# Performance work log

Measured on AMD Instinct MI355X. Metric: run time of the kernel, lower is better.

## Reference

```python
import jax, jax.numpy as jnp
import numpy as np

NUM_HEADS = 4
WINDOW = 7
DILATION = 1
NEG_MIN = jnp.finfo(jnp.float32).min


def _offsets():
    r = WINDOW // 2
    return [(i - r) * DILATION for i in range(WINDOW)]


def _gather_neighbors(x):
    # x: [B, C, H, W] -> [B, C, K, H, W] with zero padding outside bounds.
    B, C, H, W = x.shape
    offs = _offsets()
    r = (WINDOW // 2) * DILATION
    xp = jnp.pad(x, ((0, 0), (0, 0), (r, r), (r, r)))
    slices = [xp[:, :, r + dy:r + dy + H, r + dx:r + dx + W]
              for dy in offs for dx in offs]
    return jnp.stack(slices, axis=2)


def _valid_mask(H, W):
    # [K, H, W] bool: neighbor (h+dy, w+dx) is inside the image.
    offs = _offsets()
    hh = jnp.arange(H)[:, None]
    ww = jnp.arange(W)[None, :]
    masks = [((hh + dy >= 0) & (hh + dy < H) & (ww + dx >= 0) & (ww + dx < W))
             for dy in offs for dx in offs]
    return jnp.stack(masks, axis=0)


def setup_inputs() -> dict:
    key = jax.random.key(0)
    k1, k2, k3 = jax.random.split(key, 3)
    shape = (2, 64, 96, 96)
    return {
        "q": jax.random.normal(k1, shape, dtype=jnp.float32),
        "k": jax.random.normal(k2, shape, dtype=jnp.float32),
        "v": jax.random.normal(k3, shape, dtype=jnp.float32),
    }


def reference(q, k, v):
    B, C, H, W = q.shape
    d_head = C // NUM_HEADS
    K = WINDOW * WINDOW

    q_heads = q.reshape(B, NUM_HEADS, d_head, H, W)
    k_nb = _gather_neighbors(k).reshape(B, NUM_HEADS, d_head, K, H, W)
    v_nb = _gather_neighbors(v).reshape(B, NUM_HEADS, d_head, K, H, W)
    # [B, heads, K, d_head, H, W]
    k_nb = jnp.transpose(k_nb, (0, 1, 3, 2, 4, 5))
    v_nb = jnp.transpose(v_nb, (0, 1, 3, 2, 4, 5))

    scale = 1.0 / jnp.sqrt(jnp.float32(d_head))
    scores = jnp.einsum('bhdyx,bhkdyx->bhkyx', q_heads, k_nb) * scale
    mask = _valid_mask(H, W)[None, None]  # [1,1,K,H,W]
    scores = jnp.where(mask, scores, NEG_MIN)
    attn = jax.nn.softmax(scores, axis=2)
    out = jnp.einsum('bhkyx,bhkdyx->bhdyx', attn, v_nb)
    return out.reshape(B, C, H, W)
```

## Files before the change

### kernel.cpp

```cpp
#include <hip/hip_runtime.h>

#define HH 96
#define WW 96
#define CH 64
#define NHEADS 4
#define DHEAD 16
#define BATCH 2
#define PLANE (HH * WW)

#define BROWS 6
#define BCOLS 16
#define HROWS (BROWS + 6)
#define HCOLS 24
#define KPITCH 20
#define KPIX (HROWS * HCOLS)
#define KPIXA (KPIX + 8)
#define VPITCH HCOLS
#define VCH (HROWS * VPITCH + 8)
#define TY_N (HH / BROWS)
#define TX_N (WW / BCOLS)

typedef _Float16 half4 __attribute__((ext_vector_type(4)));
typedef _Float16 h2 __attribute__((ext_vector_type(2)));
typedef float f32x4 __attribute__((ext_vector_type(4)));

__device__ __forceinline__ half4 pack4(float a, float b, float c, float d) {
#if __has_builtin(__builtin_amdgcn_cvt_pkrtz)
    h2 lo = __builtin_bit_cast(h2, __builtin_amdgcn_cvt_pkrtz(a, b));
    h2 hi = __builtin_bit_cast(h2, __builtin_amdgcn_cvt_pkrtz(c, d));
    half4 r; r.x = lo.x; r.y = lo.y; r.z = hi.x; r.w = hi.y;
    return r;
#else
    half4 r; r.x = (_Float16)a; r.y = (_Float16)b;
    r.z = (_Float16)c; r.w = (_Float16)d;
    return r;
#endif
}

template <bool INTERIOR>
__device__ __forceinline__ void block_body(
    const float* __restrict__ q, const float* __restrict__ k,
    const float* __restrict__ v, float* __restrict__ out,
    _Float16* __restrict__ lk, _Float16* __restrict__ lv,
    int c0, int h0, int w0)
{
    const int tid = threadIdx.x;

    const int lane = tid & 63;
    const int wid  = tid >> 6;
    const int lp   = lane & 15;
    const int lg   = lane >> 4;
    const int h    = h0 + wid;

    const float QS = 0.25f * 1.4426950408889634f;
    const int qbase = (c0 + lg * 4) * PLANE + h * WW + w0 + lp;
    half4 qf;
    qf.x = (_Float16)(q[qbase] * QS);
    qf.y = (_Float16)(q[qbase + PLANE] * QS);
    qf.z = (_Float16)(q[qbase + 2 * PLANE] * QS);
    qf.w = (_Float16)(q[qbase + 3 * PLANE] * QS);

    const int l16  = tid & 15;
    const int grp  = tid >> 4;
    const int col0 = l16 * 2;
    const bool act = (col0 < HCOLS);

    if constexpr (INTERIOR) {
        float2 kb[8];
#pragma unroll
        for (int r = 0; r < 8; ++r) {
            const int sid = r * 24 + grp;
            const int row = sid >> 4, ch = sid & 15;
            if (act)
                kb[r] = *(const float2*)(k + (size_t)(c0 + ch) * PLANE +
                                         (h0 - 3 + row) * WW + (w0 - 4) + col0);
        }
#pragma unroll
        for (int r = 0; r < 8; ++r) {
            const int sid = r * 24 + grp;
            const int row = sid >> 4, ch = sid & 15;
            if (act) {
                const int pix = row * HCOLS + col0;
                lk[pix * KPITCH + ch]       = (_Float16)kb[r].x;
                lk[(pix + 1) * KPITCH + ch] = (_Float16)kb[r].y;
            }
        }
        float2 vb[8];
#pragma unroll
        for (int r = 0; r < 8; ++r) {
            const int sid = r * 24 + grp;
            const int row = sid >> 4, ch = sid & 15;
            if (act)
                vb[r] = *(const float2*)(v + (size_t)(c0 + ch) * PLANE +
                                         (h0 - 3 + row) * WW + (w0 - 4) + col0);
        }
#pragma unroll
        for (int r = 0; r < 8; ++r) {
            const int sid = r * 24 + grp;
            const int row = sid >> 4, ch = sid & 15;
            if (act) {
                h2 t; t.x = (_Float16)vb[r].x; t.y = (_Float16)vb[r].y;
                *(h2*)&lv[ch * VCH + row * VPITCH + col0] = t;
            }
        }
    } else {
#pragma unroll
        for (int r = 0; r < 8; ++r) {
            const int sid = r * 24 + grp;
            const int row = sid >> 4, ch = sid & 15;
            if (act) {
                const int gh = min(max(h0 - 3 + row, 0), HH - 1);
                const int ga = min(max(w0 - 4 + col0, 0), WW - 1);
                const int gb = min(max(w0 - 3 + col0, 0), WW - 1);
                const float* p0 = k + (size_t)(c0 + ch) * PLANE + gh * WW;
                const int pix = row * HCOLS + col0;
                lk[pix * KPITCH + ch]       = (_Float16)p0[ga];
                lk[(pix + 1) * KPITCH + ch] = (_Float16)p0[gb];
            }
        }
#pragma unroll
        for (int r = 0; r < 8; ++r) {
            const int sid = r * 24 + grp;
            const int row = sid >> 4, ch = sid & 15;
            if (act) {
                const int gh = min(max(h0 - 3 + row, 0), HH - 1);
                const int ga = min(max(w0 - 4 + col0, 0), WW - 1);
                const int gb = min(max(w0 - 3 + col0, 0), WW - 1);
                const float* p0 = v + (size_t)(c0 + ch) * PLANE + gh * WW;
                h2 t; t.x = (_Float16)p0[ga]; t.y = (_Float16)p0[gb];
                *(h2*)&lv[ch * VCH + row * VPITCH + col0] = t;
            }
        }
    }

    {
        h2 z; z.x = (_Float16)0.f; z.y = (_Float16)0.f;
        if (tid < 80)
            *(h2*)&lk[KPIX * KPITCH + tid * 2] = z;
        if (tid < 64)
            *(h2*)&lv[(tid >> 2) * VCH + HROWS * VPITCH + (tid & 3) * 2] = z;
    }
    __syncthreads();

    bool ok1[4], ok2[4];
#pragma unroll
    for (int e = 0; e < 4; ++e) {
        const int j1 = lg * 4 + e;
        const int j2 = 16 + j1;
        ok1[e] = ((unsigned)(j1 - lp - 1) < 7u);
        ok2[e] = ((unsigned)(j2 - lp - 1) < 7u);
        if constexpr (!INTERIOR) {
            ok1[e] = ok1[e] && ((unsigned)(w0 - 4 + j1) < (unsigned)WW);
            ok2[e] = ok2[e] && ((unsigned)(w0 - 4 + j2) < (unsigned)WW);
        }
    }

    f32x4 accA = {0.f, 0.f, 0.f, 0.f};
    f32x4 accB = {0.f, 0.f, 0.f, 0.f};
    float ssA = 0.f, ssB = 0.f;

#pragma unroll
    for (int dy = 0; dy < 7; ++dy) {
        if constexpr (!INTERIOR) {
            if ((unsigned)(h + dy - 3) >= (unsigned)HH) continue;
        }
        const int r = wid + dy;

        const half4 ka1 = *(const half4*)&lk[(r * HCOLS + lp) * KPITCH + lg * 4];
        const half4 ka2 = *(const half4*)&lk[(r * HCOLS + 16 + lp) * KPITCH + lg * 4];
        const f32x4 zz = {0.f, 0.f, 0.f, 0.f};
        f32x4 s1 = __builtin_amdgcn_mfma_f32_16x16x16f16(ka1, qf, zz, 0, 0, 0);
        f32x4 s2 = __builtin_amdgcn_mfma_f32_16x16x16f16(ka2, qf, zz, 0, 0, 0);

        const float e10 = ok1[0] ? __builtin_amdgcn_exp2f(s1[0]) : 0.f;
        const float e11 = ok1[1] ? __builtin_amdgcn_exp2f(s1[1]) : 0.f;
        const float e12 = ok1[2] ? __builtin_amdgcn_exp2f(s1[2]) : 0.f;
        const float e13 = ok1[3] ? __builtin_amdgcn_exp2f(s1[3]) : 0.f;
        const float e20 = ok2[0] ? __builtin_amdgcn_exp2f(s2[0]) : 0.f;
        const float e21 = ok2[1] ? __builtin_amdgcn_exp2f(s2[1]) : 0.f;
        const float e22 = ok2[2] ? __builtin_amdgcn_exp2f(s2[2]) : 0.f;
        const float e23 = ok2[3] ? __builtin_amdgcn_exp2f(s2[3]) : 0.f;
        ssA += (e10 + e11) + (e12 + e13);
        ssB += (e20 + e21) + (e22 + e23);
        const half4 p1 = pack4(e10, e11, e12, e13);
        const half4 p2 = pack4(e20, e21, e22, e23);

        const half4 va1 = *(const half4*)&lv[lp * VCH + r * VPITCH + lg * 4];
        const half4 va2 = *(const half4*)&lv[lp * VCH + r * VPITCH + 16 + lg * 4];
        accA = __builtin_amdgcn_mfma_f32_16x16x16f16(va1, p1, accA, 0, 0, 0);
        accB = __builtin_amdgcn_mfma_f32_16x16x16f16(va2, p2, accB, 0, 0, 0);
    }

    float ssum = ssA + ssB;
    ssum += __shfl_xor(ssum, 16, 64);
    ssum += __shfl_xor(ssum, 32, 64);
    const float inv = 1.0f / ssum;

    const f32x4 acc = accA + accB;

    const int obase = (c0 + lg * 4) * PLANE + h * WW + w0 + lp;
#pragma unroll
    for (int e = 0; e < 4; ++e)
        out[obase + e * PLANE] = acc[e] * inv;
}

__global__ __launch_bounds__(384)
__attribute__((amdgpu_waves_per_eu(5)))
void natten_mfma6b(
    const float* __restrict__ q, const float* __restrict__ k,
    const float* __restrict__ v, float* __restrict__ out)
{
    __shared__ __align__(16) _Float16 lk[KPIXA * KPITCH];
    __shared__ __align__(16) _Float16 lv[16 * VCH];

    const int bid  = (int)blockIdx.x;
    const int slab = bid & 7;
    const int t    = bid >> 3;
    const int b = slab >> 2, head = slab & 3;
    const int ty = t / TX_N, tx = t % TX_N;
    const int c0 = b * CH + head * DHEAD;
    const int h0 = ty * BROWS, w0 = tx * BCOLS;

    const bool interior = (ty >= 1) && (ty <= TY_N - 2) &&
                          (tx >= 1) && (tx <= TX_N - 2);
    if (interior)
        block_body<true >(q, k, v, out, lk, lv, c0, h0, w0);
    else
        block_body<false>(q, k, v, out, lk, lv, c0, h0, w0);
}

extern "C" void kernel_launch(void* const* d_in, const int* in_sizes, int n_in,
                              void* d_out, int out_size, void* d_ws, size_t ws_size,
                              hipStream_t stream) {
    const float* q = (const float*)d_in[0];
    const float* k = (const float*)d_in[1];
    const float* v = (const float*)d_in[2];
    float* out = (float*)d_out;

    const int grid = BATCH * NHEADS * TY_N * TX_N;
    natten_mfma6b<<<grid, 384, 0, stream>>>(q, k, v, out);
}
```

Before: 14.93 us.

## Batch global loads, fold mask into MFMA bias, split accumulators by parity

Issues all K and V global loads, plus the Q loads, before any LDS stores, so memory latency overlaps instead of serialising. The Q scaling and mask setup move after the staging code and before the barrier. The window mask becomes an additive -1000 bias fed as the MFMA accumulator input, replacing the per-element selects after exp2. The PV accumulation is split into even and odd chains to break the MFMA dependency. This raises register pressure from holding both K and V buffers, and relies on exp2 of large negative scores underflowing to zero.

```diff
diff --git a/kernel.cpp b/kernel.cpp
--- a/kernel.cpp
+++ b/kernel.cpp
@@ -45,28 +45,22 @@
     int c0, int h0, int w0)
 {
     const int tid = threadIdx.x;
-
     const int lane = tid & 63;
     const int wid  = tid >> 6;
     const int lp   = lane & 15;
     const int lg   = lane >> 4;
     const int h    = h0 + wid;
-
-    const float QS = 0.25f * 1.4426950408889634f;
     const int qbase = (c0 + lg * 4) * PLANE + h * WW + w0 + lp;
-    half4 qf;
-    qf.x = (_Float16)(q[qbase] * QS);
-    qf.y = (_Float16)(q[qbase + PLANE] * QS);
-    qf.z = (_Float16)(q[qbase + 2 * PLANE] * QS);
-    qf.w = (_Float16)(q[qbase + 3 * PLANE] * QS);
 
     const int l16  = tid & 15;
     const int grp  = tid >> 4;
     const int col0 = l16 * 2;
     const bool act = (col0 < HCOLS);
 
+    float qr0, qr1, qr2, qr3;
+
     if constexpr (INTERIOR) {
-        float2 kb[8];
+        float2 kb[8], vb[8];
 #pragma unroll
         for (int r = 0; r < 8; ++r) {
             const int sid = r * 24 + grp;
@@ -79,21 +73,24 @@
         for (int r = 0; r < 8; ++r) {
             const int sid = r * 24 + grp;
             const int row = sid >> 4, ch = sid & 15;
+            if (act)
+                vb[r] = *(const float2*)(v + (size_t)(c0 + ch) * PLANE +
+                                         (h0 - 3 + row) * WW + (w0 - 4) + col0);
+        }
+        qr0 = q[qbase];
+        qr1 = q[qbase + PLANE];
+        qr2 = q[qbase + 2 * PLANE];
+        qr3 = q[qbase + 3 * PLANE];
+#pragma unroll
+        for (int r = 0; r < 8; ++r) {
+            const int sid = r * 24 + grp;
+            const int row = sid >> 4, ch = sid & 15;
             if (act) {
                 const int pix = row * HCOLS + col0;
                 lk[pix * KPITCH + ch]       = (_Float16)kb[r].x;
                 lk[(pix + 1) * KPITCH + ch] = (_Float16)kb[r].y;
             }
         }
-        float2 vb[8];
-#pragma unroll
-        for (int r = 0; r < 8; ++r) {
-            const int sid = r * 24 + grp;
-            const int row = sid >> 4, ch = sid & 15;
-            if (act)
-                vb[r] = *(const float2*)(v + (size_t)(c0 + ch) * PLANE +
-                                         (h0 - 3 + row) * WW + (w0 - 4) + col0);
-        }
 #pragma unroll
         for (int r = 0; r < 8; ++r) {
             const int sid = r * 24 + grp;
@@ -104,6 +101,10 @@
             }
         }
     } else {
+        qr0 = q[qbase];
+        qr1 = q[qbase + PLANE];
+        qr2 = q[qbase + 2 * PLANE];
+        qr3 = q[qbase + 3 * PLANE];
 #pragma unroll
         for (int r = 0; r < 8; ++r) {
             const int sid = r * 24 + grp;
@@ -140,23 +141,32 @@
         if (tid < 64)
             *(h2*)&lv[(tid >> 2) * VCH + HROWS * VPITCH + (tid & 3) * 2] = z;
     }
-    __syncthreads();
-
-    bool ok1[4], ok2[4];
+
+    const float QS = 0.25f * 1.4426950408889634f;
+    half4 qf;
+    qf.x = (_Float16)(qr0 * QS);
+    qf.y = (_Float16)(qr1 * QS);
+    qf.z = (_Float16)(qr2 * QS);
+    qf.w = (_Float16)(qr3 * QS);
+
+    f32x4 bias1, bias2;
 #pragma unroll
     for (int e = 0; e < 4; ++e) {
         const int j1 = lg * 4 + e;
         const int j2 = 16 + j1;
-        ok1[e] = ((unsigned)(j1 - lp - 1) < 7u);
-        ok2[e] = ((unsigned)(j2 - lp - 1) < 7u);
+        bool o1 = ((unsigned)(j1 - lp - 1) < 7u);
+        bool o2 = ((unsigned)(j2 - lp - 1) < 7u);
         if constexpr (!INTERIOR) {
-            ok1[e] = ok1[e] && ((unsigned)(w0 - 4 + j1) < (unsigned)WW);
-            ok2[e] = ok2[e] && ((unsigned)(w0 - 4 + j2) < (unsigned)WW);
-        }
-    }
-
-    f32x4 accA = {0.f, 0.f, 0.f, 0.f};
-    f32x4 accB = {0.f, 0.f, 0.f, 0.f};
+            o1 = o1 && ((unsigned)(w0 - 4 + j1) < (unsigned)WW);
+            o2 = o2 && ((unsigned)(w0 - 4 + j2) < (unsigned)WW);
+        }
+        bias1[e] = o1 ? 0.f : -1000.f;
+        bias2[e] = o2 ? 0.f : -1000.f;
+    }
+    __syncthreads();
+
+    f32x4 accAe = {0.f, 0.f, 0.f, 0.f}, accAo = {0.f, 0.f, 0.f, 0.f};
+    f32x4 accBe = {0.f, 0.f, 0.f, 0.f}, accBo = {0.f, 0.f, 0.f, 0.f};
     float ssA = 0.f, ssB = 0.f;
 
 #pragma unroll
@@ -168,18 +178,17 @@
 
         const half4 ka1 = *(const half4*)&lk[(r * HCOLS + lp) * KPITCH + lg * 4];
         const half4 ka2 = *(const half4*)&lk[(r * HCOLS + 16 + lp) * KPITCH + lg * 4];
-        const f32x4 zz = {0.f, 0.f, 0.f, 0.f};
-        f32x4 s1 = __builtin_amdgcn_mfma_f32_16x16x16f16(ka1, qf, zz, 0, 0, 0);
-        f32x4 s2 = __builtin_amdgcn_mfma_f32_16x16x16f16(ka2, qf, zz, 0, 0, 0);
-
-        const float e10 = ok1[0] ? __builtin_amdgcn_exp2f(s1[0]) : 0.f;
-        const float e11 = ok1[1] ? __builtin_amdgcn_exp2f(s1[1]) : 0.f;
-        const float e12 = ok1[2] ? __builtin_amdgcn_exp2f(s1[2]) : 0.f;
-        const float e13 = ok1[3] ? __builtin_amdgcn_exp2f(s1[3]) : 0.f;
-        const float e20 = ok2[0] ? __builtin_amdgcn_exp2f(s2[0]) : 0.f;
-        const float e21 = ok2[1] ? __builtin_amdgcn_exp2f(s2[1]) : 0.f;
-        const float e22 = ok2[2] ? __builtin_amdgcn_exp2f(s2[2]) : 0.f;
-        const float e23 = ok2[3] ? __builtin_amdgcn_exp2f(s2[3]) : 0.f;
+        f32x4 s1 = __builtin_amdgcn_mfma_f32_16x16x16f16(ka1, qf, bias1, 0, 0, 0);
+        f32x4 s2 = __builtin_amdgcn_mfma_f32_16x16x16f16(ka2, qf, bias2, 0, 0, 0);
+
+        const float e10 = __builtin_amdgcn_exp2f(s1[0]);
+        const float e11 = __builtin_amdgcn_exp2f(s1[1]);
+        const float e12 = __builtin_amdgcn_exp2f(s1[2]);
+        const float e13 = __builtin_amdgcn_exp2f(s1[3]);
+        const float e20 = __builtin_amdgcn_exp2f(s2[0]);
+        const float e21 = __builtin_amdgcn_exp2f(s2[1]);
+        const float e22 = __builtin_amdgcn_exp2f(s2[2]);
+        const float e23 = __builtin_amdgcn_exp2f(s2[3]);
         ssA += (e10 + e11) + (e12 + e13);
         ssB += (e20 + e21) + (e22 + e23);
         const half4 p1 = pack4(e10, e11, e12, e13);
@@ -187,8 +196,13 @@
 
         const half4 va1 = *(const half4*)&lv[lp * VCH + r * VPITCH + lg * 4];
         const half4 va2 = *(const half4*)&lv[lp * VCH + r * VPITCH + 16 + lg * 4];
-        accA = __builtin_amdgcn_mfma_f32_16x16x16f16(va1, p1, accA, 0, 0, 0);
-        accB = __builtin_amdgcn_mfma_f32_16x16x16f16(va2, p2, accB, 0, 0, 0);
+        if (dy & 1) {
+            accAo = __builtin_amdgcn_mfma_f32_16x16x16f16(va1, p1, accAo, 0, 0, 0);
+            accBo = __builtin_amdgcn_mfma_f32_16x16x16f16(va2, p2, accBo, 0, 0, 0);
+        } else {
+            accAe = __builtin_amdgcn_mfma_f32_16x16x16f16(va1, p1, accAe, 0, 0, 0);
+            accBe = __builtin_amdgcn_mfma_f32_16x16x16f16(va2, p2, accBe, 0, 0, 0);
+        }
     }
 
     float ssum = ssA + ssB;
@@ -196,7 +210,7 @@
     ssum += __shfl_xor(ssum, 32, 64);
     const float inv = 1.0f / ssum;
 
-    const f32x4 acc = accA + accB;
+    const f32x4 acc = (accAe + accAo) + (accBe + accBo);
 
     const int obase = (c0 + lg * 4) * PLANE + h * WW + w0 + lp;
 #pragma unroll
@@ -206,7 +220,7 @@
 
 __global__ __launch_bounds__(384)
 __attribute__((amdgpu_waves_per_eu(5)))
-void natten_mfma6b(
+void natten_mfma6c(
     const float* __restrict__ q, const float* __restrict__ k,
     const float* __restrict__ v, float* __restrict__ out)
 {
@@ -238,5 +252,5 @@
     float* out = (float*)d_out;
 
     const int grid = BATCH * NHEADS * TY_N * TX_N;
-    natten_mfma6b<<<grid, 384, 0, stream>>>(q, k, v, out);
-}
+    natten_mfma6c<<<grid, 384, 0, stream>>>(q, k, v, out);
+}
```

Measured after the change: 16.25 us. 1.09x slower.
